# Optimization experiments

Hardware: AMD Instinct MI355X
Metric: run time of the kernel (lower is better)

## Reference

```python
import jax, jax.numpy as jnp
import numpy as np

LN_EPS = 1e-5

def setup_inputs() -> dict:
    key = jax.random.key(0)
    k0, k1, k2, k3 = jax.random.split(key, 4)
    B, N, D = 4, 4096, 512
    x = jax.random.normal(k0, (B, N, D), dtype=jnp.float32)
    s = 1.0 / np.sqrt(D)
    Wq = jax.random.normal(k1, (D, D), dtype=jnp.float32) * s
    Wk = jax.random.normal(k2, (D, D), dtype=jnp.float32) * s
    Wv = jax.random.normal(k3, (D, D), dtype=jnp.float32) * s
    gamma = jnp.ones((D,), dtype=jnp.float32)
    beta = jnp.zeros((D,), dtype=jnp.float32)
    return {"x": x, "Wq": Wq, "Wk": Wk, "Wv": Wv, "gamma": gamma, "beta": beta}

def reference(x, Wq, Wk, Wv, gamma, beta):
    # x: [B, N, D]
    D = x.shape[-1]
    q = jnp.einsum('bnd,de->bne', x, Wq)
    k = jnp.einsum('bnd,de->bne', x, Wk)
    v = jnp.einsum('bnd,de->bne', x, Wv)
    # full [B, N, N] score matrix, as in the original bmm chain
    dist = jnp.einsum('bne,bme->bnm', q, k) * (1.0 / jnp.sqrt(jnp.float32(D)))
    dist = jax.nn.softmax(dist, axis=-1)
    att = jnp.einsum('bnm,bmd->bnd', dist, v)
    # residual + LayerNorm over last dim
    h = att + x
    mu = jnp.mean(h, axis=-1, keepdims=True)
    var = jnp.mean(jnp.square(h - mu), axis=-1, keepdims=True)
    out = (h - mu) * jax.lax.rsqrt(var + LN_EPS) * gamma + beta
    return out
```

## Files before the change

### kernel.cpp

```cpp
#include <hip/hip_runtime.h>
#include <stdint.h>

typedef __attribute__((ext_vector_type(8))) __bf16 bf16x8;
typedef __attribute__((ext_vector_type(4))) float f32x4;
typedef __attribute__((ext_vector_type(16))) float f32x16;
typedef unsigned short u16;
typedef unsigned char u8;
typedef unsigned int u32;
typedef long i64;

#define LN_EPS 1e-5f

__device__ __forceinline__ float bf2f(u16 u){
  union { u32 i; float f; } v; v.i = ((u32)u) << 16; return v.f;
}
__device__ __forceinline__ u16 f2bf(float f){
  union { float f; u32 i; } v; v.f = f;
  u32 u = v.i;
  u += 0x7fffu + ((u >> 16) & 1u);
  return (u16)(u >> 16);
}
__device__ __forceinline__ u32 cvt_pk_fp8(float a, float b){
  u32 pk;
  asm("v_cvt_pk_fp8_f32 %0, %1, %2" : "=v"(pk) : "v"(a), "v"(b));
  return pk;
}

__device__ __forceinline__ void gload_lds16(const void* g, void* l) {
  __builtin_amdgcn_global_load_lds(
      (const __attribute__((address_space(1))) void*)g,
      (__attribute__((address_space(3))) void*)l, 16, 0, 0);
}

__global__ void xcast_kernel(const float* __restrict__ X, u16* __restrict__ Xb) {
  int idx = (blockIdx.x * 256 + threadIdx.x) * 8;
  float4 f0 = *(const float4*)&X[idx];
  float4 f1 = *(const float4*)&X[idx + 4];
  ushort4 lo, hi;
  lo.x = f2bf(f0.x); lo.y = f2bf(f0.y); lo.z = f2bf(f0.z); lo.w = f2bf(f0.w);
  hi.x = f2bf(f1.x); hi.y = f2bf(f1.y); hi.z = f2bf(f1.z); hi.w = f2bf(f1.w);
  *(ushort4*)&Xb[idx] = lo;
  *(ushort4*)&Xb[idx + 4] = hi;
}

__global__ void transpose_w_kernel(const float* __restrict__ Wq,
                                   const float* __restrict__ Wk,
                                   const float* __restrict__ Wv,
                                   u16* __restrict__ Wt) {
  const float* W = (blockIdx.y == 0) ? Wq : ((blockIdx.y == 1) ? Wk : Wv);
  u16* o = Wt + blockIdx.y * 512 * 512;
  int idx = blockIdx.x * 256 + threadIdx.x;
  int e = idx >> 9, d = idx & 511;
  o[e * 512 + d] = f2bf(W[d * 512 + e]);
}

__launch_bounds__(256, 4)
__global__ void qkv_gemm_kernel(const u16* __restrict__ Xb,
                                const u16* __restrict__ Wt,
                                u8* __restrict__ Qo,
                                u8* __restrict__ Ko,
                                u8* __restrict__ Vto8) {
  const int z = blockIdx.y;
  const u16* Wtm = Wt + z * 512 * 512;
  const int mblk = blockIdx.x & 127;
  const int nblk = blockIdx.x >> 7;
  const int m0 = mblk * 128, n0 = nblk * 128;

  __shared__ __align__(16) u8 As[128 * 64];
  __shared__ __align__(16) u8 Bs[128 * 64];

  const int tid = threadIdx.x;
  const int lane = tid & 63, w = tid >> 6;
  const int wr = w >> 1, wc = w & 1;
  const int lrow = lane & 15, quad = lane >> 4;

  f32x4 acc[4][4];
#pragma unroll
  for (int i = 0; i < 4; i++)
#pragma unroll
    for (int j = 0; j < 4; j++) acc[i][j] = (f32x4){0.f, 0.f, 0.f, 0.f};

  const int srow = lane >> 2;
  const int spos = lane & 3;

#pragma unroll
  for (int r2 = 0; r2 < 2; r2++) {
    int rowb = w * 32 + r2 * 16;
    int row = rowb + srow;
    int g = spos ^ (row & 3);
    gload_lds16(&Xb[(m0 + row) * 512 + g * 8], &As[rowb * 64]);
    gload_lds16(&Wtm[(n0 + row) * 512 + g * 8], &Bs[rowb * 64]);
  }

  for (int k = 0; k < 16; k++) {
    __syncthreads();
    bf16x8 a[4], b[4];
#pragma unroll
    for (int t = 0; t < 4; t++) {
      int ra = wr * 64 + t * 16 + lrow;
      a[t] = *(const bf16x8*)&As[ra * 64 + (quad ^ (ra & 3)) * 16];
      int rb = wc * 64 + t * 16 + lrow;
      b[t] = *(const bf16x8*)&Bs[rb * 64 + (quad ^ (rb & 3)) * 16];
    }
    __syncthreads();
    if (k < 15) {
      int k0n = (k + 1) * 32;
#pragma unroll
      for (int r2 = 0; r2 < 2; r2++) {
        int rowb = w * 32 + r2 * 16;
        int row = rowb + srow;
        int g = spos ^ (row & 3);
        gload_lds16(&Xb[(m0 + row) * 512 + k0n + g * 8], &As[rowb * 64]);
        gload_lds16(&Wtm[(n0 + row) * 512 + k0n + g * 8], &Bs[rowb * 64]);
      }
    }
#pragma unroll
    for (int i = 0; i < 4; i++)
#pragma unroll
      for (int j = 0; j < 4; j++)
        acc[i][j] = __builtin_amdgcn_mfma_f32_16x16x32_bf16(a[i], b[j], acc[i][j], 0, 0, 0);
  }

  if (z < 2) {
    u8* O = (z == 0) ? Qo : Ko;
#pragma unroll
    for (int i = 0; i < 4; i++) {
      int rbase = m0 + wr * 64 + i * 16 + quad * 4;
#pragma unroll
      for (int j = 0; j < 4; j++) {
        int col = n0 + wc * 64 + j * 16 + lrow;
        u32 pk01 = cvt_pk_fp8(acc[i][j][0], acc[i][j][1]);
        u32 pk23 = cvt_pk_fp8(acc[i][j][2], acc[i][j][3]);
        O[(rbase + 0) * 512 + col] = (u8)pk01;
        O[(rbase + 1) * 512 + col] = (u8)(pk01 >> 8);
        O[(rbase + 2) * 512 + col] = (u8)pk23;
        O[(rbase + 3) * 512 + col] = (u8)(pk23 >> 8);
      }
    }
  } else {
#pragma unroll
    for (int i = 0; i < 4; i++) {
      int rbase = m0 + wr * 64 + i * 16 + quad * 4;
#pragma unroll
      for (int j = 0; j < 4; j++) {
        int col = n0 + wc * 64 + j * 16 + lrow;
        u32 pk01 = cvt_pk_fp8(acc[i][j][0], acc[i][j][1]);
        u32 pk23 = cvt_pk_fp8(acc[i][j][2], acc[i][j][3]);
        u32 pk = (pk01 & 0xffffu) | (pk23 << 16);
        *(u32*)&Vto8[col * 16384 + rbase] = pk;
      }
    }
  }
}

template <int NSPLIT>
__launch_bounds__(256, 2)
__global__ void attn_partial_kernel(const u8* __restrict__ Q,
                                    const u8* __restrict__ K,
                                    const u8* __restrict__ Vt8,
                                    u16* __restrict__ Opart,
                                    float* __restrict__ L) {
  constexpr int SPAN = 4096 / NSPLIT;
  constexpr int ITERS = SPAN / 32;
  const int b = blockIdx.y;
  const int split = blockIdx.z;
  const int q0 = blockIdx.x * 64;
  const int tid = threadIdx.x;
  const int lane = tid & 63, w = tid >> 6;
  const int lrow = lane & 15, quad = lane >> 4;
  const int l31 = lane & 31, half = lane >> 5;

  __shared__ __align__(16) u8 Ks8[32 * 512];
  __shared__ __align__(16) u8 Vs8[512 * 32];
  __shared__ __align__(16) u8 Pb8[64 * 40];

  const int keybase = b * 4096 + split * SPAN;

  const int qtok = b * 4096 + q0 + w * 16 + lrow;
  i64 qf[16];
#pragma unroll
  for (int s = 0; s < 16; s++)
    qf[s] = *(const i64*)&Q[qtok * 512 + s * 32 + quad * 8];

  f32x16 Oacc[2][4];
#pragma unroll
  for (int i = 0; i < 2; i++)
#pragma unroll
    for (int j = 0; j < 4; j++)
#pragma unroll
      for (int e = 0; e < 16; e++) Oacc[i][j][e] = 0.f;

  float lsum[4] = {0.f, 0.f, 0.f, 0.f};
  const float scale = 0.044194173824159216f;

#pragma unroll
  for (int i = 0; i < 4; i++) {
    int row = w * 8 + i * 2 + (lane >> 5);
    int g = (lane & 31) ^ (row & 7);
    gload_lds16(&K[(keybase + row) * 512 + g * 16], &Ks8[(w * 8 + i * 2) * 512]);
  }
#pragma unroll
  for (int run = 0; run < 4; run++) {
    int rowb = w * 128 + run * 32;
    int n = rowb + (lane >> 1);
    int g16 = (lane & 1) ^ ((n >> 2) & 1);
    gload_lds16(&Vt8[n * 16384 + keybase + g16 * 16], &Vs8[rowb * 32]);
  }

  for (int it = 0; it < ITERS; ++it) {
    __syncthreads();

    f32x4 S0 = {0.f, 0.f, 0.f, 0.f}, S1 = {0.f, 0.f, 0.f, 0.f};
#pragma unroll
    for (int s = 0; s < 16; s++) {
      int gs = (2 * s + (quad >> 1)) ^ (lrow & 7);
      int off = gs * 16 + (quad & 1) * 8;
      i64 k0 = *(const i64*)&Ks8[lrow * 512 + off];
      i64 k1 = *(const i64*)&Ks8[(16 + lrow) * 512 + off];
      S0 = __builtin_amdgcn_mfma_f32_16x16x32_fp8_fp8(qf[s], k0, S0, 0, 0, 0);
      S1 = __builtin_amdgcn_mfma_f32_16x16x32_fp8_fp8(qf[s], k1, S1, 0, 0, 0);
    }

#pragma unroll
    for (int r = 0; r < 4; r++) {
      float p0 = __expf(S0[r] * scale);
      float p1 = __expf(S1[r] * scale);
      lsum[r] += p0 + p1;
      u32 pk = cvt_pk_fp8(p0, p1);
      int prow = w * 16 + quad * 4 + r;
      Pb8[prow * 40 + lrow] = (u8)pk;
      Pb8[prow * 40 + 16 + lrow] = (u8)(pk >> 8);
    }

    __syncthreads();

    const int kknext = (it + 1) * 32;
    if (it < ITERS - 1) {
#pragma unroll
      for (int i = 0; i < 4; i++) {
        int row = w * 8 + i * 2 + (lane >> 5);
        int g = (lane & 31) ^ (row & 7);
        gload_lds16(&K[(keybase + kknext + row) * 512 + g * 16],
                    &Ks8[(w * 8 + i * 2) * 512]);
      }
    }

    i64 af[2][2];
#pragma unroll
    for (int i = 0; i < 2; i++)
#pragma unroll
      for (int kg = 0; kg < 2; kg++)
        af[i][kg] = *(const i64*)&Pb8[(i * 32 + l31) * 40 + kg * 16 + half * 8];

    i64 bv[4][2];
#pragma unroll
    for (int j = 0; j < 4; j++) {
      int n = w * 128 + j * 32 + l31;
      int x = (n >> 2) & 1;
#pragma unroll
      for (int kg = 0; kg < 2; kg++)
        bv[j][kg] = *(const i64*)&Vs8[n * 32 + (kg ^ x) * 16 + half * 8];
    }

    asm volatile("s_waitcnt lgkmcnt(0)" ::: "memory");

    if (it < ITERS - 1) {
#pragma unroll
      for (int run = 0; run < 4; run++) {
        int rowb = w * 128 + run * 32;
        int n = rowb + (lane >> 1);
        int g16 = (lane & 1) ^ ((n >> 2) & 1);
        gload_lds16(&Vt8[n * 16384 + keybase + kknext + g16 * 16], &Vs8[rowb * 32]);
      }
    }

#pragma unroll
    for (int j = 0; j < 4; j++)
#pragma unroll
      for (int i = 0; i < 2; i++) {
        Oacc[i][j] = __builtin_amdgcn_mfma_f32_32x32x16_fp8_fp8(af[i][0], bv[j][0], Oacc[i][j], 0, 0, 0);
        Oacc[i][j] = __builtin_amdgcn_mfma_f32_32x32x16_fp8_fp8(af[i][1], bv[j][1], Oacc[i][j], 0, 0, 0);
      }
  }

#pragma unroll
  for (int r = 0; r < 4; r++) {
    float s = lsum[r];
    s += __shfl_xor(s, 1); s += __shfl_xor(s, 2);
    s += __shfl_xor(s, 4); s += __shfl_xor(s, 8);
    lsum[r] = s;
  }
  const int tokw = b * 4096 + q0 + w * 16 + quad * 4;
  if (lrow == 0) {
#pragma unroll
    for (int r = 0; r < 4; r++)
      L[split * 16384 + tokw + r] = lsum[r];
  }

  u16* Ob = Opart + (size_t)split * (16384u * 512u);
  const int tokbase = b * 4096 + q0;
#pragma unroll
  for (int i = 0; i < 2; i++)
#pragma unroll
    for (int j = 0; j < 4; j++) {
      int col = w * 128 + j * 32 + l31;
#pragma unroll
      for (int p = 0; p < 16; p++) {
        int row = i * 32 + (p & 3) + 8 * (p >> 2) + 4 * half;
        Ob[(tokbase + row) * 512 + col] = f2bf(Oacc[i][j][p]);
      }
    }
}

template <int NSPLIT>
__launch_bounds__(256)
__global__ void combine_ln_kernel(const u16* __restrict__ Opart,
                                  const float* __restrict__ L,
                                  const float* __restrict__ X,
                                  const float* __restrict__ gamma,
                                  const float* __restrict__ beta,
                                  float* __restrict__ Out) {
  const int lane = threadIdx.x & 63;
  const int tok = blockIdx.x * 4 + (threadIdx.x >> 6);
  float lt = 0.f;
#pragma unroll
  for (int s = 0; s < NSPLIT; s++) lt += L[s * 16384 + tok];
  const float inv_l = 1.f / lt;
  const int base = tok * 512 + lane * 8;

  float h[8] = {0.f, 0.f, 0.f, 0.f, 0.f, 0.f, 0.f, 0.f};
#pragma unroll
  for (int s = 0; s < NSPLIT; s++) {
    uint4 avec = *(const uint4*)&Opart[(size_t)s * (16384u * 512u) + base];
    const u16* ap = (const u16*)&avec;
#pragma unroll
    for (int i = 0; i < 8; i++) h[i] += bf2f(ap[i]);
  }

  float4 x0 = *(const float4*)&X[base];
  float4 x1 = *(const float4*)&X[base + 4];
  float xs[8] = {x0.x, x0.y, x0.z, x0.w, x1.x, x1.y, x1.z, x1.w};
#pragma unroll
  for (int i = 0; i < 8; i++) h[i] = h[i] * inv_l + xs[i];

  float sum = 0.f, sq = 0.f;
#pragma unroll
  for (int i = 0; i < 8; i++) { sum += h[i]; sq += h[i] * h[i]; }
#pragma unroll
  for (int d = 1; d < 64; d <<= 1) {
    sum += __shfl_xor(sum, d);
    sq  += __shfl_xor(sq, d);
  }
  float mu = sum * (1.f / 512.f);
  float var = sq * (1.f / 512.f) - mu * mu;
  float rstd = rsqrtf(var + LN_EPS);

  float4 g0 = *(const float4*)&gamma[lane * 8];
  float4 g1 = *(const float4*)&gamma[lane * 8 + 4];
  float4 b0 = *(const float4*)&beta[lane * 8];
  float4 b1 = *(const float4*)&beta[lane * 8 + 4];
  float gs[8] = {g0.x, g0.y, g0.z, g0.w, g1.x, g1.y, g1.z, g1.w};
  float bs[8] = {b0.x, b0.y, b0.z, b0.w, b1.x, b1.y, b1.z, b1.w};

  float4 o0, o1;
  float* op = (float*)&o0;
#pragma unroll
  for (int i = 0; i < 4; i++) op[i] = (h[i] - mu) * rstd * gs[i] + bs[i];
  float* op1 = (float*)&o1;
#pragma unroll
  for (int i = 0; i < 4; i++) op1[i] = (h[i + 4] - mu) * rstd * gs[i + 4] + bs[i + 4];
  *(float4*)&Out[base] = o0;
  *(float4*)&Out[base + 4] = o1;
}

extern "C" void kernel_launch(void* const* d_in, const int* in_sizes, int n_in,
                              void* d_out, int out_size, void* d_ws, size_t ws_size,
                              hipStream_t stream) {
  const float* x = (const float*)d_in[0];
  const float* Wq = (const float*)d_in[1];
  const float* Wk = (const float*)d_in[2];
  const float* Wv = (const float*)d_in[3];
  const float* gamma = (const float*)d_in[4];
  const float* beta = (const float*)d_in[5];

  char* ws = (char*)d_ws;
  u8*  Qws   = (u8*)(ws);
  u8*  Kws   = (u8*)(ws + 8388608);
  u8*  Vt8ws = (u8*)(ws + 16777216);
  u16* Wtws  = (u16*)(ws + 25165824);
  u16* Xbws  = (u16*)(ws + 26738688);
  u16* Opws  = (u16*)(ws + 26738688);

  const size_t PART = 16777216;
  const size_t need4 = 26738688 + 4 * PART + 4 * 16384 * sizeof(float);
  const int nsplit = (ws_size >= need4) ? 4 : 2;
  float* Lws = (float*)(ws + 26738688 + (size_t)nsplit * PART);

  hipLaunchKernelGGL(xcast_kernel, dim3(4096), dim3(256), 0, stream, x, Xbws);
  hipLaunchKernelGGL(transpose_w_kernel, dim3(1024, 3), dim3(256), 0, stream,
                     Wq, Wk, Wv, Wtws);
  hipLaunchKernelGGL(qkv_gemm_kernel, dim3(512, 3), dim3(256), 0, stream,
                     Xbws, Wtws, Qws, Kws, Vt8ws);
  if (nsplit == 4) {
    hipLaunchKernelGGL(HIP_KERNEL_NAME(attn_partial_kernel<4>),
                       dim3(64, 4, 4), dim3(256), 0, stream,
                       Qws, Kws, Vt8ws, Opws, Lws);
    hipLaunchKernelGGL(HIP_KERNEL_NAME(combine_ln_kernel<4>),
                       dim3(4096), dim3(256), 0, stream,
                       Opws, Lws, x, gamma, beta, (float*)d_out);
  } else {
    hipLaunchKernelGGL(HIP_KERNEL_NAME(attn_partial_kernel<2>),
                       dim3(64, 4, 2), dim3(256), 0, stream,
                       Qws, Kws, Vt8ws, Opws, Lws);
    hipLaunchKernelGGL(HIP_KERNEL_NAME(combine_ln_kernel<2>),
                       dim3(4096), dim3(256), 0, stream,
                       Opws, Lws, x, gamma, beta, (float*)d_out);
  }
}
```

Before: 280.1 us.

## Double-buffer K/V tiles and keep P in registers via shuffles in attention

The attention kernel now double-buffers the K and V LDS tiles, prefetching the next tile right after the loop-top barrier. It also drops the shared P buffer and second barrier by computing transposed scores (K as A operand) and redistributing FP8 probabilities across lanes with shuffles. The PV product becomes 32 16x16x32 MFMAs per wave covering all 512 output columns for the wave's 16 queries, instead of 32x32 tiles split by column. The split count is fixed at 2. This doubles LDS use and raises accumulator registers per thread, which may reduce occupancy, and all four waves now read the whole V tile.

```diff
diff --git a/kernel.cpp b/kernel.cpp
--- a/kernel.cpp
+++ b/kernel.cpp
@@ -3,10 +3,10 @@
 
 typedef __attribute__((ext_vector_type(8))) __bf16 bf16x8;
 typedef __attribute__((ext_vector_type(4))) float f32x4;
-typedef __attribute__((ext_vector_type(16))) float f32x16;
 typedef unsigned short u16;
 typedef unsigned char u8;
 typedef unsigned int u32;
+typedef unsigned long long u64;
 typedef long i64;
 
 #define LN_EPS 1e-5f
@@ -168,11 +168,9 @@
   const int tid = threadIdx.x;
   const int lane = tid & 63, w = tid >> 6;
   const int lrow = lane & 15, quad = lane >> 4;
-  const int l31 = lane & 31, half = lane >> 5;
-
-  __shared__ __align__(16) u8 Ks8[32 * 512];
-  __shared__ __align__(16) u8 Vs8[512 * 32];
-  __shared__ __align__(16) u8 Pb8[64 * 40];
+
+  __shared__ __align__(16) u8 Ks8[2][32 * 512];
+  __shared__ __align__(16) u8 Vs8[2][512 * 32];
 
   const int keybase = b * 4096 + split * SPAN;
 
@@ -182,134 +180,101 @@
   for (int s = 0; s < 16; s++)
     qf[s] = *(const i64*)&Q[qtok * 512 + s * 32 + quad * 8];
 
-  f32x16 Oacc[2][4];
-#pragma unroll
-  for (int i = 0; i < 2; i++)
-#pragma unroll
-    for (int j = 0; j < 4; j++)
-#pragma unroll
-      for (int e = 0; e < 16; e++) Oacc[i][j][e] = 0.f;
-
-  float lsum[4] = {0.f, 0.f, 0.f, 0.f};
+  f32x4 Oacc[32];
+#pragma unroll
+  for (int j = 0; j < 32; j++) Oacc[j] = (f32x4){0.f, 0.f, 0.f, 0.f};
+
+  float lsum = 0.f;
   const float scale = 0.044194173824159216f;
 
-#pragma unroll
-  for (int i = 0; i < 4; i++) {
-    int row = w * 8 + i * 2 + (lane >> 5);
-    int g = (lane & 31) ^ (row & 7);
-    gload_lds16(&K[(keybase + row) * 512 + g * 16], &Ks8[(w * 8 + i * 2) * 512]);
-  }
-#pragma unroll
-  for (int run = 0; run < 4; run++) {
-    int rowb = w * 128 + run * 32;
-    int n = rowb + (lane >> 1);
-    int g16 = (lane & 1) ^ ((n >> 2) & 1);
-    gload_lds16(&Vt8[n * 16384 + keybase + g16 * 16], &Vs8[rowb * 32]);
-  }
+  auto stageK = [&](int kk, u8* Kbuf) {
+#pragma unroll
+    for (int i = 0; i < 4; i++) {
+      int row = w * 8 + i * 2 + (lane >> 5);
+      int g = (lane & 31) ^ (row & 7);
+      gload_lds16(&K[(keybase + kk + row) * 512 + g * 16],
+                  &Kbuf[(w * 8 + i * 2) * 512]);
+    }
+  };
+  auto stageV = [&](int kk, u8* Vbuf) {
+#pragma unroll
+    for (int run = 0; run < 4; run++) {
+      int rowb = w * 128 + run * 32;
+      int n = rowb + (lane >> 1);
+      int g16 = (lane & 1) ^ ((n >> 2) & 1);
+      gload_lds16(&Vt8[n * 16384 + keybase + kk + g16 * 16], &Vbuf[rowb * 32]);
+    }
+  };
+
+  stageK(0, Ks8[0]);
+  stageV(0, Vs8[0]);
 
   for (int it = 0; it < ITERS; ++it) {
+    const int cur = it & 1;
+    const u8* Ksc = Ks8[cur];
+    const u8* Vsc = Vs8[cur];
+
     __syncthreads();
+    if (it < ITERS - 1) {
+      stageK((it + 1) * 32, Ks8[cur ^ 1]);
+      stageV((it + 1) * 32, Vs8[cur ^ 1]);
+    }
 
     f32x4 S0 = {0.f, 0.f, 0.f, 0.f}, S1 = {0.f, 0.f, 0.f, 0.f};
 #pragma unroll
     for (int s = 0; s < 16; s++) {
       int gs = (2 * s + (quad >> 1)) ^ (lrow & 7);
       int off = gs * 16 + (quad & 1) * 8;
-      i64 k0 = *(const i64*)&Ks8[lrow * 512 + off];
-      i64 k1 = *(const i64*)&Ks8[(16 + lrow) * 512 + off];
-      S0 = __builtin_amdgcn_mfma_f32_16x16x32_fp8_fp8(qf[s], k0, S0, 0, 0, 0);
-      S1 = __builtin_amdgcn_mfma_f32_16x16x32_fp8_fp8(qf[s], k1, S1, 0, 0, 0);
-    }
-
-#pragma unroll
-    for (int r = 0; r < 4; r++) {
-      float p0 = __expf(S0[r] * scale);
-      float p1 = __expf(S1[r] * scale);
-      lsum[r] += p0 + p1;
-      u32 pk = cvt_pk_fp8(p0, p1);
-      int prow = w * 16 + quad * 4 + r;
-      Pb8[prow * 40 + lrow] = (u8)pk;
-      Pb8[prow * 40 + 16 + lrow] = (u8)(pk >> 8);
-    }
-
-    __syncthreads();
-
-    const int kknext = (it + 1) * 32;
-    if (it < ITERS - 1) {
-#pragma unroll
-      for (int i = 0; i < 4; i++) {
-        int row = w * 8 + i * 2 + (lane >> 5);
-        int g = (lane & 31) ^ (row & 7);
-        gload_lds16(&K[(keybase + kknext + row) * 512 + g * 16],
-                    &Ks8[(w * 8 + i * 2) * 512]);
+      i64 k0 = *(const i64*)&Ksc[lrow * 512 + off];
+      i64 k1 = *(const i64*)&Ksc[(16 + lrow) * 512 + off];
+      S0 = __builtin_amdgcn_mfma_f32_16x16x32_fp8_fp8(k0, qf[s], S0, 0, 0, 0);
+      S1 = __builtin_amdgcn_mfma_f32_16x16x32_fp8_fp8(k1, qf[s], S1, 0, 0, 0);
+    }
+
+    float p00 = __expf(S0[0] * scale), p01 = __expf(S0[1] * scale);
+    float p02 = __expf(S0[2] * scale), p03 = __expf(S0[3] * scale);
+    float p10 = __expf(S1[0] * scale), p11 = __expf(S1[1] * scale);
+    float p12 = __expf(S1[2] * scale), p13 = __expf(S1[3] * scale);
+    lsum += ((p00 + p01) + (p02 + p03)) + ((p10 + p11) + (p12 + p13));
+    u32 dwA = (cvt_pk_fp8(p00, p01) & 0xffffu) | (cvt_pk_fp8(p02, p03) << 16);
+    u32 dwB = (cvt_pk_fp8(p10, p11) & 0xffffu) | (cvt_pk_fp8(p12, p13) << 16);
+
+    {
+      int srcl = lrow + 32 * (quad & 1);
+      u32 loA = (u32)__shfl((int)dwA, srcl);
+      u32 hiA = (u32)__shfl((int)dwA, srcl + 16);
+      u32 loB = (u32)__shfl((int)dwB, srcl);
+      u32 hiB = (u32)__shfl((int)dwB, srcl + 16);
+      u32 lo = (quad >= 2) ? loB : loA;
+      u32 hi = (quad >= 2) ? hiB : hiA;
+      i64 af = (i64)(((u64)hi << 32) | (u64)lo);
+
+#pragma unroll
+      for (int j = 0; j < 32; j++) {
+        int n = j * 16 + lrow;
+        int off = (((quad >> 1) ^ ((n >> 2) & 1)) << 4) + (quad & 1) * 8;
+        i64 bv = *(const i64*)&Vsc[n * 32 + off];
+        Oacc[j] = __builtin_amdgcn_mfma_f32_16x16x32_fp8_fp8(af, bv, Oacc[j], 0, 0, 0);
       }
     }
-
-    i64 af[2][2];
-#pragma unroll
-    for (int i = 0; i < 2; i++)
-#pragma unroll
-      for (int kg = 0; kg < 2; kg++)
-        af[i][kg] = *(const i64*)&Pb8[(i * 32 + l31) * 40 + kg * 16 + half * 8];
-
-    i64 bv[4][2];
-#pragma unroll
-    for (int j = 0; j < 4; j++) {
-      int n = w * 128 + j * 32 + l31;
-      int x = (n >> 2) & 1;
-#pragma unroll
-      for (int kg = 0; kg < 2; kg++)
-        bv[j][kg] = *(const i64*)&Vs8[n * 32 + (kg ^ x) * 16 + half * 8];
-    }
-
-    asm volatile("s_waitcnt lgkmcnt(0)" ::: "memory");
-
-    if (it < ITERS - 1) {
-#pragma unroll
-      for (int run = 0; run < 4; run++) {
-        int rowb = w * 128 + run * 32;
-        int n = rowb + (lane >> 1);
-        int g16 = (lane & 1) ^ ((n >> 2) & 1);
-        gload_lds16(&Vt8[n * 16384 + keybase + kknext + g16 * 16], &Vs8[rowb * 32]);
-      }
-    }
-
-#pragma unroll
-    for (int j = 0; j < 4; j++)
-#pragma unroll
-      for (int i = 0; i < 2; i++) {
-        Oacc[i][j] = __builtin_amdgcn_mfma_f32_32x32x16_fp8_fp8(af[i][0], bv[j][0], Oacc[i][j], 0, 0, 0);
-        Oacc[i][j] = __builtin_amdgcn_mfma_f32_32x32x16_fp8_fp8(af[i][1], bv[j][1], Oacc[i][j], 0, 0, 0);
-      }
-  }
-
-#pragma unroll
-  for (int r = 0; r < 4; r++) {
-    float s = lsum[r];
-    s += __shfl_xor(s, 1); s += __shfl_xor(s, 2);
-    s += __shfl_xor(s, 4); s += __shfl_xor(s, 8);
-    lsum[r] = s;
-  }
-  const int tokw = b * 4096 + q0 + w * 16 + quad * 4;
-  if (lrow == 0) {
-#pragma unroll
-    for (int r = 0; r < 4; r++)
-      L[split * 16384 + tokw + r] = lsum[r];
+  }
+
+  {
+    float s = lsum;
+    s += __shfl_xor(s, 16);
+    s += __shfl_xor(s, 32);
+    if (quad == 0)
+      L[split * 16384 + b * 4096 + q0 + w * 16 + lrow] = s;
   }
 
   u16* Ob = Opart + (size_t)split * (16384u * 512u);
-  const int tokbase = b * 4096 + q0;
-#pragma unroll
-  for (int i = 0; i < 2; i++)
-#pragma unroll
-    for (int j = 0; j < 4; j++) {
-      int col = w * 128 + j * 32 + l31;
-#pragma unroll
-      for (int p = 0; p < 16; p++) {
-        int row = i * 32 + (p & 3) + 8 * (p >> 2) + 4 * half;
-        Ob[(tokbase + row) * 512 + col] = f2bf(Oacc[i][j][p]);
-      }
-    }
+  const int tokr = b * 4096 + q0 + w * 16 + quad * 4;
+#pragma unroll
+  for (int j = 0; j < 32; j++) {
+#pragma unroll
+    for (int p = 0; p < 4; p++)
+      Ob[(size_t)(tokr + p) * 512 + j * 16 + lrow] = f2bf(Oacc[j][p]);
+  }
 }
 
 template <int NSPLIT>
@@ -390,30 +355,18 @@
   u16* Wtws  = (u16*)(ws + 25165824);
   u16* Xbws  = (u16*)(ws + 26738688);
   u16* Opws  = (u16*)(ws + 26738688);
-
   const size_t PART = 16777216;
-  const size_t need4 = 26738688 + 4 * PART + 4 * 16384 * sizeof(float);
-  const int nsplit = (ws_size >= need4) ? 4 : 2;
-  float* Lws = (float*)(ws + 26738688 + (size_t)nsplit * PART);
+  float* Lws = (float*)(ws + 26738688 + 2 * PART);
 
   hipLaunchKernelGGL(xcast_kernel, dim3(4096), dim3(256), 0, stream, x, Xbws);
   hipLaunchKernelGGL(transpose_w_kernel, dim3(1024, 3), dim3(256), 0, stream,
                      Wq, Wk, Wv, Wtws);
   hipLaunchKernelGGL(qkv_gemm_kernel, dim3(512, 3), dim3(256), 0, stream,
                      Xbws, Wtws, Qws, Kws, Vt8ws);
-  if (nsplit == 4) {
-    hipLaunchKernelGGL(HIP_KERNEL_NAME(attn_partial_kernel<4>),
-                       dim3(64, 4, 4), dim3(256), 0, stream,
-                       Qws, Kws, Vt8ws, Opws, Lws);
-    hipLaunchKernelGGL(HIP_KERNEL_NAME(combine_ln_kernel<4>),
-                       dim3(4096), dim3(256), 0, stream,
-                       Opws, Lws, x, gamma, beta, (float*)d_out);
-  } else {
-    hipLaunchKernelGGL(HIP_KERNEL_NAME(attn_partial_kernel<2>),
-                       dim3(64, 4, 2), dim3(256), 0, stream,
-                       Qws, Kws, Vt8ws, Opws, Lws);
-    hipLaunchKernelGGL(HIP_KERNEL_NAME(combine_ln_kernel<2>),
-                       dim3(4096), dim3(256), 0, stream,
-                       Opws, Lws, x, gamma, beta, (float*)d_out);
-  }
-}
+  hipLaunchKernelGGL(HIP_KERNEL_NAME(attn_partial_kernel<2>),
+                     dim3(64, 4, 2), dim3(256), 0, stream,
+                     Qws, Kws, Vt8ws, Opws, Lws);
+  hipLaunchKernelGGL(HIP_KERNEL_NAME(combine_ln_kernel<2>),
+                     dim3(4096), dim3(256), 0, stream,
+                     Opws, Lws, x, gamma, beta, (float*)d_out);
+}
```

New measurement: 295.7 us. 5.6% more time.
